# Kernel optimization log

Hardware: AMD Instinct MI355X
Metric: run time of the kernel (lower is better)

The kernel has to match this reference:

```python
import jax, jax.numpy as jnp
import numpy as np


def setup_inputs() -> dict:
    key = jax.random.key(0)
    ks = jax.random.split(key, 8)
    N, C, T, V = 32, 64, 256, 25
    OUT, INTER, S = 64, 16, 3
    W_SCALE = 0.05  # keep complex softmax exp() well-conditioned
    return {
        "x_real": jax.random.normal(ks[0], (N, C, T, V), jnp.float32),
        "x_imag": jax.random.normal(ks[1], (N, C, T, V), jnp.float32),
        "A": jax.random.uniform(ks[2], (S, V, V), jnp.float32),
        "PA": jax.random.normal(ks[3], (S, V, V), jnp.float32) * 1e-3,
        "Wa": jax.random.normal(ks[4], (S, 2 * INTER, 2 * C), jnp.float32) * W_SCALE,
        "ba": jnp.zeros((S, 2 * INTER), jnp.float32),
        "Wb": jax.random.normal(ks[5], (S, 2 * INTER, 2 * C), jnp.float32) * W_SCALE,
        "bb": jnp.zeros((S, 2 * INTER), jnp.float32),
        "Wd": jax.random.normal(ks[6], (S, 2 * OUT, 2 * C), jnp.float32) * W_SCALE,
        "bd": jnp.zeros((S, 2 * OUT), jnp.float32),
        "bn_weight": jnp.ones((OUT,), jnp.float32),
        "bn_bias": jnp.zeros((OUT,), jnp.float32),
    }


def _cconv1x1(z, W, b):
    # C_Conv2d with k=1: 1x1 conv over concat(real, imag) channels.
    zc = jnp.concatenate([z.real, z.imag], axis=1)          # [N, 2*Cin, T, V]
    o = jnp.einsum("oc,nctv->notv", W, zc) + b[None, :, None, None]
    h = W.shape[0] // 2
    return jax.lax.complex(o[:, :h], o[:, h:])              # [N, Cout, T, V] complex


def _forward(x_real, x_imag, A, PA, Wa, ba, Wb, bb, Wd, bd, bn_weight, bn_bias):
    x = jax.lax.complex(x_real, x_imag)                     # [N, C, T, V]
    N, C, T, V = x.shape
    inter = Wa.shape[1] // 2
    Afull = A + PA                                          # [3, V, V] real
    X2 = x.reshape(N, C * T, V)
    y = None
    for i in range(A.shape[0]):
        A1 = _cconv1x1(x, Wa[i], ba[i])                     # [N, inter, T, V]
        A1 = A1.transpose(0, 3, 1, 2).reshape(N, V, inter * T)
        A2 = _cconv1x1(x, Wb[i], bb[i]).reshape(N, inter * T, V)
        S = jnp.matmul(A1, A2) / (inter * T)                # [N, V, V] complex
        # complex softmax over dim=1 (no max-subtraction, faithful to C_softmax)
        ez = jnp.exp(S)
        S = ez / jnp.sum(ez, axis=1, keepdims=True)
        S = S + Afull[i]
        z = jnp.matmul(X2, S).reshape(N, C, T, V)
        z = _cconv1x1(z, Wd[i], bd[i])                      # [N, OUT, T, V]
        y = z if y is None else y + z
    # C_BatchNorm2d on complex input: complex mean, real variance = E|y-mu|^2
    mu = jnp.mean(y, axis=(0, 2, 3))                        # [OUT] complex
    var = jnp.mean(jnp.abs(y - mu[None, :, None, None]) ** 2, axis=(0, 2, 3))
    yn = (y - mu[None, :, None, None]) / jnp.sqrt(var + 1e-5)[None, :, None, None]
    yn = yn * bn_weight[None, :, None, None] + bn_bias[None, :, None, None]
    yn = yn + x  # down = identity (in_channels == out_channels)
    return jnp.stack([yn.real, yn.imag])                    # [2, N, OUT, T, V] real


def reference(x_real, x_imag, A, PA, Wa, ba, Wb, bb, Wd, bd, bn_weight, bn_bias):
    return _forward(x_real, x_imag, A, PA, Wa, ba, Wb, bb, Wd, bd, bn_weight, bn_bias)
```

## Files before the change

kernel.cpp:

```cpp
#include <hip/hip_runtime.h>
#include <hip/hip_bf16.h>
#include <stdint.h>

#define NN 32
#define CC 64
#define TTOT 256
#define VV 25
#define NS 3
constexpr int TV  = TTOT * VV;
constexpr int CTV = CC * TV;
constexpr size_t PLANE = (size_t)NN * CTV;

typedef unsigned short ushort_t;
using short8 = __attribute__((ext_vector_type(8))) short;
using f32x4  = __attribute__((ext_vector_type(4))) float;

static __device__ __forceinline__ ushort_t f2bf(float f) {
  __hip_bfloat16 h = __float2bfloat16(f);
  return reinterpret_cast<ushort_t&>(h);
}
static __device__ __forceinline__ float bf2f(ushort_t h) {
  union { uint32_t u; float f; } v; v.u = ((uint32_t)h) << 16;
  return v.f;
}
static __device__ __forceinline__ int SWZ(int row, int k) {
  return ((row << 7) + k) ^ ((row & 7) << 3);
}
static __device__ __forceinline__ int SWZ64(int row, int k) {
  return ((row << 6) + k) ^ ((row & 7) << 3);
}
static __device__ __forceinline__ f32x4 mfma16(short8 a, short8 b, f32x4 c) {
  return __builtin_amdgcn_mfma_f32_16x16x32_bf16(a, b, c, 0, 0, 0);
}
static __device__ __forceinline__ short8 negbf8(short8 x) {
  short8 r;
#pragma unroll
  for (int j = 0; j < 8; ++j) r[j] = x[j] ^ (short)0x8000;
  return r;
}

__global__ __launch_bounds__(256) void k0_wfrag(
    const float* __restrict__ Wd, const float* __restrict__ Wa,
    const float* __restrict__ Wb, ushort_t* __restrict__ wfrag,
    ushort_t* __restrict__ wab)
{
  const int i = blockIdx.x;
  for (int e = threadIdx.x; e < 16384; e += 256) {
    int ot = e >> 11, m = (e >> 9) & 3, l = (e >> 3) & 63, j = e & 7;
    int r  = ot * 16 + (l & 15);
    int c = m * 16 + ((l >> 4) << 2) + (j >> 1), comp = j & 1;
    wfrag[(size_t)i * 16384 + e] = f2bf(Wd[(size_t)i * 16384 + r * 128 + comp * 64 + c]);
  }
  for (int e = threadIdx.x; e < 8192; e += 256) {
    int mt = e >> 11, ks = (e >> 9) & 3, l = (e >> 3) & 63, j = e & 7;
    int r  = mt * 16 + (l & 15);
    int kp = ks * 32 + ((l >> 4) << 3) + j;
    float v = (r < 32) ? Wa[((size_t)i * 32 + r) * 128 + kp]
                       : Wb[((size_t)i * 32 + (r - 32)) * 128 + kp];
    wab[(size_t)i * 8192 + e] = f2bf(v);
  }
}

__global__ __launch_bounds__(256) void k1_spart(
    const float* __restrict__ xr, const float* __restrict__ xi,
    const ushort_t* __restrict__ wab, const float* __restrict__ ba,
    const float* __restrict__ bb, float* __restrict__ Spart)
{
  const int tc = blockIdx.x, n = blockIdx.y;
  const int tid = threadIdx.x, lane = tid & 63, wv = tid >> 6;
  const int r16 = lane & 15, gw = lane >> 4;
  __shared__ alignas(16) ushort_t zc[128 * 128];
  __shared__ alignas(16) ushort_t Ga[32 * 128];
  __shared__ alignas(16) ushort_t Gb[32 * 128];

  for (int e4 = tid; e4 < 128 * 25; e4 += 256) {
    int c = e4 / 25, q = e4 % 25;
    const float* src = (c < 64) ? xr : xi;
    float4 w = *(const float4*)&src[(size_t)n * CTV + (c & 63) * TV + tc * 100 + q * 4];
#pragma unroll
    for (int jj = 0; jj < 4; ++jj) {
      int g = q * 4 + jj, t = g / 25, v = g - t * 25;
      zc[SWZ(t * 32 + v, c)] = f2bf(((const float*)&w)[jj]);
    }
  }
  for (int e = tid; e < 28 * 128; e += 256) {
    int r7 = e >> 7, c = e & 127;
    int t = r7 / 7, vv = 25 + r7 % 7;
    zc[SWZ(t * 32 + vv, c)] = 0;
  }

  const int mu = wv >> 1, nv = wv & 1;

  for (int i = 0; i < NS; ++i) {
    __syncthreads();

    {
      short8 afr[4];
#pragma unroll
      for (int ks = 0; ks < 4; ++ks)
        afr[ks] = *(const short8*)&wab[((((size_t)i * 4 + wv) * 4 + ks) * 64 + lane) * 8];
      float bias[4];
#pragma unroll
      for (int j = 0; j < 4; ++j) {
        int row = wv * 16 + gw * 4 + j;
        bias[j] = (row < 32) ? ba[i * 32 + row] : bb[i * 32 + (row - 32)];
      }
      ushort_t* gbuf = (wv < 2) ? Ga : Gb;
      const int half = (wv & 1) * 64;
      for (int nt = 0; nt < 8; ++nt) {
        f32x4 acc = {0.f, 0.f, 0.f, 0.f};
        const int brow = nt * 16 + r16;
#pragma unroll
        for (int ks = 0; ks < 4; ++ks) {
          short8 bfr = *(const short8*)&zc[SWZ(brow, ks * 32 + gw * 8)];
          acc = mfma16(afr[ks], bfr, acc);
        }
        int pos2 = nt * 16 + r16;
        int t = pos2 >> 5, v = pos2 & 31;
        int k0w = half + t * 16 + gw * 4;
        uint32_t w0 = (uint32_t)f2bf(acc[0] + bias[0]) | ((uint32_t)f2bf(acc[1] + bias[1]) << 16);
        uint32_t w1 = (uint32_t)f2bf(acc[2] + bias[2]) | ((uint32_t)f2bf(acc[3] + bias[3]) << 16);
        uint2 pk; pk.x = w0; pk.y = w1;
        *(uint2*)&gbuf[SWZ(v, k0w)] = pk;
      }
    }
    __syncthreads();

    {
      const int urow = mu * 16 + r16;
      const int vrow = nv * 16 + r16;
      f32x4 Prr = {0.f,0.f,0.f,0.f}, Pii = {0.f,0.f,0.f,0.f};
      f32x4 Pri = {0.f,0.f,0.f,0.f}, Pir = {0.f,0.f,0.f,0.f};
#pragma unroll
      for (int ks = 0; ks < 2; ++ks) {
        int ko = ks * 32 + gw * 8;
        short8 arF = *(const short8*)&Ga[SWZ(urow, ko)];
        short8 aiF = *(const short8*)&Ga[SWZ(urow, 64 + ko)];
        short8 brF = *(const short8*)&Gb[SWZ(vrow, ko)];
        short8 biF = *(const short8*)&Gb[SWZ(vrow, 64 + ko)];
        Prr = mfma16(arF, brF, Prr);
        Pii = mfma16(aiF, biF, Pii);
        Pri = mfma16(arF, biF, Pri);
        Pir = mfma16(aiF, brF, Pir);
      }
#pragma unroll
      for (int j = 0; j < 4; ++j) {
        int u = mu * 16 + gw * 4 + j;
        int v = nv * 16 + r16;
        if (u < VV && v < VV) {
          size_t idx = ((((size_t)i * NN + n) * 64 + tc) * 625 + u * 25 + v) * 2;
          Spart[idx]     = Prr[j] - Pii[j];
          Spart[idx + 1] = Pri[j] + Pir[j];
        }
      }
    }
  }
}

__global__ __launch_bounds__(256) void k2_softmax(
    const float* __restrict__ Spart, const float* __restrict__ Aw,
    const float* __restrict__ PA, ushort_t* __restrict__ sfrag)
{
  const int i = blockIdx.x, n = blockIdx.y, tid = threadIdx.x;
  __shared__ float ez[625 * 2];
  __shared__ float den[25 * 2];
  for (int e = tid; e < 625; e += 256) {
    float sr = 0.f, si = 0.f;
    const float* p = Spart + (((size_t)i * NN + n) * 64 * 625 + e) * 2;
    for (int tcb = 0; tcb < 64; ++tcb) { sr += p[0]; si += p[1]; p += 625 * 2; }
    sr *= (1.f / 4096.f); si *= (1.f / 4096.f);
    float m = expf(sr);
    ez[e * 2] = m * cosf(si);
    ez[e * 2 + 1] = m * sinf(si);
  }
  __syncthreads();
  if (tid < 25) {
    float dr = 0.f, di = 0.f;
    for (int u = 0; u < 25; ++u) { dr += ez[(u * 25 + tid) * 2]; di += ez[(u * 25 + tid) * 2 + 1]; }
    float inv = 1.f / (dr * dr + di * di);
    den[tid * 2] = dr * inv; den[tid * 2 + 1] = -di * inv;
  }
  __syncthreads();
  for (int e = tid; e < 625; e += 256) {
    int v = e % 25;
    float er = ez[e * 2], ei = ez[e * 2 + 1];
    float dr = den[v * 2], di = den[v * 2 + 1];
    float outr = er * dr - ei * di + Aw[i * 625 + e] + PA[i * 625 + e];
    float outi = er * di + ei * dr;
    ez[e * 2] = outr; ez[e * 2 + 1] = outi;
  }
  __syncthreads();
  for (int e = tid; e < 256; e += 256) {
    int l = e & 63, nt = (e >> 6) & 1, m = e >> 7;
    int u0 = (l >> 4) << 3, v = nt * 16 + (l & 15);
    short8 pk;
#pragma unroll
    for (int j = 0; j < 8; ++j) {
      int u = u0 + j;
      float val = 0.f;
      if (u < VV && v < VV)
        val = (m == 0) ? ez[(u * 25 + v) * 2] : ez[(u * 25 + v) * 2 + 1];
      pk[j] = (short)f2bf(val);
    }
    *(short8*)&sfrag[((size_t)(i * NN + n) * 256 + e) * 8] = pk;
  }
}

__global__ __launch_bounds__(256, 4) void k3_y(
    const float* __restrict__ xr, const float* __restrict__ xi,
    const ushort_t* __restrict__ sfrag, const ushort_t* __restrict__ wfrag,
    const float* __restrict__ bd, float* __restrict__ out,
    float* __restrict__ bnpart)
{
  const int tq2 = blockIdx.x, n = blockIdx.y;
  const int tid = threadIdx.x, lane = tid & 63, wv = tid >> 6;
  const int r16 = lane & 15, gw = lane >> 4;
  const int tl = wv >> 1, h = wv & 1;
  __shared__ alignas(16) ushort_t xs[128 * 64];
  __shared__ float stats[4][64][2];

  for (int e2 = tid; e2 < 128 * 25; e2 += 256) {
    int c = e2 / 25, q = e2 % 25;
    const float* src = (c < 64) ? xr : xi;
    float2 w = *(const float2*)&src[(size_t)n * CTV + (size_t)(c & 63) * TV + tq2 * 50 + q * 2];
    int g0 = q * 2, g1 = g0 + 1;
    int t0 = g0 / 25, u0 = g0 - t0 * 25;
    int t1 = g1 / 25, u1 = g1 - t1 * 25;
    xs[SWZ64(c, t0 * 32 + u0)] = f2bf(w.x);
    xs[SWZ64(c, t1 * 32 + u1)] = f2bf(w.y);
  }
  for (int e = tid; e < 128 * 14; e += 256) {
    int c = e / 14, r = e % 14;
    int t = r / 7, u = 25 + r % 7;
    xs[SWZ64(c, t * 32 + u)] = 0;
  }
  __syncthreads();

  const int kx = tl * 32 + gw * 8;

  f32x4 acc[4][2];
#pragma unroll
  for (int a = 0; a < 4; ++a) { acc[a][0] = {0.f,0.f,0.f,0.f}; acc[a][1] = {0.f,0.f,0.f,0.f}; }

#pragma unroll 1
  for (int i = 0; i < NS; ++i) {
    const ushort_t* sb = sfrag + (size_t)(i * NN + n) * 2048;
    short8 sf[2][2];
#pragma unroll
    for (int m = 0; m < 2; ++m)
#pragma unroll
      for (int nt = 0; nt < 2; ++nt)
        sf[m][nt] = *(const short8*)&sb[((m * 2 + nt) * 64 + lane) * 8];

    const ushort_t* wbase = wfrag + (size_t)i * 16384;
    short8 wcur[4], wnxt[4];
#pragma unroll
    for (int m = 0; m < 4; ++m)
      wcur[m] = *(const short8*)&wbase[(size_t)(((h * 4 + 0) * 4 + m) * 64 + lane) * 8];

    short8 snI[2];
#pragma unroll
    for (int nt = 0; nt < 2; ++nt) snI[nt] = negbf8(sf[1][nt]);
    short8 bp[4][2];
#pragma unroll
    for (int tile = 0; tile < 4; ++tile) {
      short8 axr_ = *(const short8*)&xs[SWZ64(tile * 16 + r16, kx)];
      short8 axi_ = *(const short8*)&xs[SWZ64(64 + tile * 16 + r16, kx)];
#pragma unroll
      for (int nt = 0; nt < 2; ++nt) {
        f32x4 zr = {0.f,0.f,0.f,0.f}, zi = {0.f,0.f,0.f,0.f};
        zr = mfma16(axr_, sf[0][nt], zr);
        zr = mfma16(axi_, snI[nt], zr);
        zi = mfma16(axr_, sf[1][nt], zi);
        zi = mfma16(axi_, sf[0][nt], zi);
        short8 pk;
#pragma unroll
        for (int j = 0; j < 4; ++j) {
          pk[2 * j]     = (short)f2bf(zr[j]);
          pk[2 * j + 1] = (short)f2bf(zi[j]);
        }
        bp[tile][nt] = pk;
      }
    }

#pragma unroll
    for (int ot = 0; ot < 4; ++ot) {
      if (ot < 3) {
#pragma unroll
        for (int m = 0; m < 4; ++m)
          wnxt[m] = *(const short8*)&wbase[(size_t)(((h * 4 + ot + 1) * 4 + m) * 64 + lane) * 8];
      }
#pragma unroll
      for (int m = 0; m < 4; ++m) {
        acc[ot][0] = mfma16(wcur[m], bp[m][0], acc[ot][0]);
        acc[ot][1] = mfma16(wcur[m], bp[m][1], acc[ot][1]);
      }
#pragma unroll
      for (int m = 0; m < 4; ++m) wcur[m] = wnxt[m];
    }
  }

  const int t = tq2 * 2 + tl;
#pragma unroll
  for (int ot = 0; ot < 4; ++ot) {
#pragma unroll
    for (int j = 0; j < 4; ++j) {
      int lrow = ot * 16 + gw * 4 + j;
      int row = h * 64 + lrow;
      float bias = bd[row] + bd[128 + row] + bd[256 + row];
      float s = 0.f, q = 0.f;
#pragma unroll
      for (int nt = 0; nt < 2; ++nt) {
        int v = nt * 16 + r16;
        float val = acc[ot][nt][j] + bias;
        if (v < VV) {
          out[(size_t)(row >> 6) * PLANE + (size_t)n * CTV + (row & 63) * TV + t * VV + v] = val;
          s += val; q += val * val;
        }
      }
#pragma unroll
      for (int d = 1; d < 16; d <<= 1) { s += __shfl_xor(s, d); q += __shfl_xor(q, d); }
      if (r16 == 0) { stats[wv][lrow][0] = s; stats[wv][lrow][1] = q; }
    }
  }
  __syncthreads();
  if (tid < 128) {
    int hh = tid >> 6, lr = tid & 63;
    float s = stats[hh][lr][0] + stats[2 + hh][lr][0];
    float q = stats[hh][lr][1] + stats[2 + hh][lr][1];
    size_t b = (size_t)n * 128 + tq2;
    bnpart[(b * 128 + tid) * 2]     = s;
    bnpart[(b * 128 + tid) * 2 + 1] = q;
  }
}

__global__ __launch_bounds__(256) void k4_stats(
    const float* __restrict__ bnpart, const float* __restrict__ bnw,
    const float* __restrict__ bnb, float* __restrict__ coeff)
{
  const int o = blockIdx.x, tid = threadIdx.x;
  float sr = 0.f, qr = 0.f, si = 0.f, qi = 0.f;
  for (int b = tid; b < 4096; b += 256) {
    const float* p = bnpart + ((size_t)b * 128 + o) * 2;
    sr += p[0]; qr += p[1];
    const float* p2 = bnpart + ((size_t)b * 128 + 64 + o) * 2;
    si += p2[0]; qi += p2[1];
  }
#pragma unroll
  for (int d = 1; d < 64; d <<= 1) {
    sr += __shfl_xor(sr, d); qr += __shfl_xor(qr, d);
    si += __shfl_xor(si, d); qi += __shfl_xor(qi, d);
  }
  __shared__ float red[4][4];
  int lane = tid & 63, wv = tid >> 6;
  if (lane == 0) { red[wv][0] = sr; red[wv][1] = qr; red[wv][2] = si; red[wv][3] = qi; }
  __syncthreads();
  if (tid == 0) {
    sr = red[0][0] + red[1][0] + red[2][0] + red[3][0];
    qr = red[0][1] + red[1][1] + red[2][1] + red[3][1];
    si = red[0][2] + red[1][2] + red[2][2] + red[3][2];
    qi = red[0][3] + red[1][3] + red[2][3] + red[3][3];
    const float invM = 1.f / (float)((size_t)NN * TTOT * VV);
    float mur = sr * invM, mui = si * invM;
    float var = (qr + qi) * invM - mur * mur - mui * mui;
    float inv = rsqrtf(var + 1e-5f);
    coeff[o * 4 + 0] = mur; coeff[o * 4 + 1] = mui;
    coeff[o * 4 + 2] = inv * bnw[o]; coeff[o * 4 + 3] = bnb[o];
  }
}

__global__ __launch_bounds__(256) void k5_norm(
    const float* __restrict__ xr, const float* __restrict__ xi,
    const float* __restrict__ coeff, float* __restrict__ out)
{
  size_t idx0 = ((size_t)blockIdx.x * 256 + threadIdx.x) * 4;
  size_t stride = (size_t)gridDim.x * 256 * 4;
  for (size_t e = idx0; e < PLANE; e += stride) {
    int o = (int)((e / TV) & 63);
    float4 cf = *(const float4*)&coeff[o * 4];
    float4 yr = *(float4*)&out[e];
    float4 yi = *(float4*)&out[PLANE + e];
    float4 vr = *(const float4*)&xr[e];
    float4 vi = *(const float4*)&xi[e];
    yr.x = (yr.x - cf.x) * cf.z + cf.w + vr.x;
    yr.y = (yr.y - cf.x) * cf.z + cf.w + vr.y;
    yr.z = (yr.z - cf.x) * cf.z + cf.w + vr.z;
    yr.w = (yr.w - cf.x) * cf.z + cf.w + vr.w;
    yi.x = (yi.x - cf.y) * cf.z + vi.x;
    yi.y = (yi.y - cf.y) * cf.z + vi.y;
    yi.z = (yi.z - cf.y) * cf.z + vi.z;
    yi.w = (yi.w - cf.y) * cf.z + vi.w;
    *(float4*)&out[e] = yr;
    *(float4*)&out[PLANE + e] = yi;
  }
}

extern "C" void kernel_launch(void* const* d_in, const int* in_sizes, int n_in,
                              void* d_out, int out_size, void* d_ws, size_t ws_size,
                              hipStream_t stream) {
  const float* xr  = (const float*)d_in[0];
  const float* xi  = (const float*)d_in[1];
  const float* Aw  = (const float*)d_in[2];
  const float* PA  = (const float*)d_in[3];
  const float* Wa  = (const float*)d_in[4];
  const float* ba  = (const float*)d_in[5];
  const float* Wb  = (const float*)d_in[6];
  const float* bb  = (const float*)d_in[7];
  const float* Wd  = (const float*)d_in[8];
  const float* bd  = (const float*)d_in[9];
  const float* bnw = (const float*)d_in[10];
  const float* bnb = (const float*)d_in[11];
  float* out = (float*)d_out;
  float* ws = (float*)d_ws;

  float*    Spart  = ws;
  float*    bnpart = ws;
  ushort_t* sfrag  = (ushort_t*)(ws + 7680000);
  ushort_t* wfrag  = (ushort_t*)(ws + 7778304);
  ushort_t* wab    = (ushort_t*)(ws + 7802880);
  float*    coeff  = ws + 7815168;

  k0_wfrag<<<NS, 256, 0, stream>>>(Wd, Wa, Wb, wfrag, wab);
  k1_spart<<<dim3(64, NN), 256, 0, stream>>>(xr, xi, wab, ba, bb, Spart);
  k2_softmax<<<dim3(NS, NN), 256, 0, stream>>>(Spart, Aw, PA, sfrag);
  k3_y<<<dim3(128, NN), 256, 0, stream>>>(xr, xi, sfrag, wfrag, bd, out, bnpart);
  k4_stats<<<64, 256, 0, stream>>>(bnpart, bnw, bnb, coeff);
  k5_norm<<<6400, 256, 0, stream>>>(xr, xi, coeff, out);
}
```

Measured before the change: 263.8 us.

## Make k3 persistent over 8 timesteps with LDS-resident weights and double-buffered x

k3_y now runs 512-thread blocks, each covering 8 timesteps in four chunks of two instead of one block per two timesteps. The Wd fragments for all three subsets are staged once in LDS, and x chunks are prefetched into registers and written to double-buffered LDS so global loads overlap the MFMA work. k1_spart is also restructured to compute all three subsets' Ga/Gb projections before a single barrier, replacing the per-subset barrier pairs at the cost of three times the LDS for those buffers. The larger LDS footprint and register pressure may lower occupancy, and grid parallelism drops fourfold.

```diff
diff --git a/kernel.cpp b/kernel.cpp
--- a/kernel.cpp
+++ b/kernel.cpp
@@ -26,9 +26,6 @@
 static __device__ __forceinline__ int SWZ(int row, int k) {
   return ((row << 7) + k) ^ ((row & 7) << 3);
 }
-static __device__ __forceinline__ int SWZ64(int row, int k) {
-  return ((row << 6) + k) ^ ((row & 7) << 3);
-}
 static __device__ __forceinline__ f32x4 mfma16(short8 a, short8 b, f32x4 c) {
   return __builtin_amdgcn_mfma_f32_16x16x32_bf16(a, b, c, 0, 0, 0);
 }
@@ -70,8 +67,8 @@
   const int tid = threadIdx.x, lane = tid & 63, wv = tid >> 6;
   const int r16 = lane & 15, gw = lane >> 4;
   __shared__ alignas(16) ushort_t zc[128 * 128];
-  __shared__ alignas(16) ushort_t Ga[32 * 128];
-  __shared__ alignas(16) ushort_t Gb[32 * 128];
+  __shared__ alignas(16) ushort_t Ga[NS][32 * 128];
+  __shared__ alignas(16) ushort_t Gb[NS][32 * 128];
 
   for (int e4 = tid; e4 < 128 * 25; e4 += 256) {
     int c = e4 / 25, q = e4 % 25;
@@ -88,70 +85,68 @@
     int t = r7 / 7, vv = 25 + r7 % 7;
     zc[SWZ(t * 32 + vv, c)] = 0;
   }
+  __syncthreads();
+
+#pragma unroll 1
+  for (int i = 0; i < NS; ++i) {
+    short8 afr[4];
+#pragma unroll
+    for (int ks = 0; ks < 4; ++ks)
+      afr[ks] = *(const short8*)&wab[((((size_t)i * 4 + wv) * 4 + ks) * 64 + lane) * 8];
+    float bias[4];
+#pragma unroll
+    for (int j = 0; j < 4; ++j) {
+      int row = wv * 16 + gw * 4 + j;
+      bias[j] = (row < 32) ? ba[i * 32 + row] : bb[i * 32 + (row - 32)];
+    }
+    ushort_t* gbuf = (wv < 2) ? Ga[i] : Gb[i];
+    const int half = (wv & 1) * 64;
+    for (int nt = 0; nt < 8; ++nt) {
+      f32x4 acc = {0.f, 0.f, 0.f, 0.f};
+      const int brow = nt * 16 + r16;
+#pragma unroll
+      for (int ks = 0; ks < 4; ++ks) {
+        short8 bfr = *(const short8*)&zc[SWZ(brow, ks * 32 + gw * 8)];
+        acc = mfma16(afr[ks], bfr, acc);
+      }
+      int pos2 = nt * 16 + r16;
+      int t = pos2 >> 5, v = pos2 & 31;
+      int k0w = half + t * 16 + gw * 4;
+      uint32_t w0 = (uint32_t)f2bf(acc[0] + bias[0]) | ((uint32_t)f2bf(acc[1] + bias[1]) << 16);
+      uint32_t w1 = (uint32_t)f2bf(acc[2] + bias[2]) | ((uint32_t)f2bf(acc[3] + bias[3]) << 16);
+      uint2 pk; pk.x = w0; pk.y = w1;
+      *(uint2*)&gbuf[SWZ(v, k0w)] = pk;
+    }
+  }
+  __syncthreads();
 
   const int mu = wv >> 1, nv = wv & 1;
-
+  const int urow = mu * 16 + r16;
+  const int vrow = nv * 16 + r16;
+#pragma unroll 1
   for (int i = 0; i < NS; ++i) {
-    __syncthreads();
-
-    {
-      short8 afr[4];
-#pragma unroll
-      for (int ks = 0; ks < 4; ++ks)
-        afr[ks] = *(const short8*)&wab[((((size_t)i * 4 + wv) * 4 + ks) * 64 + lane) * 8];
-      float bias[4];
-#pragma unroll
-      for (int j = 0; j < 4; ++j) {
-        int row = wv * 16 + gw * 4 + j;
-        bias[j] = (row < 32) ? ba[i * 32 + row] : bb[i * 32 + (row - 32)];
-      }
-      ushort_t* gbuf = (wv < 2) ? Ga : Gb;
-      const int half = (wv & 1) * 64;
-      for (int nt = 0; nt < 8; ++nt) {
-        f32x4 acc = {0.f, 0.f, 0.f, 0.f};
-        const int brow = nt * 16 + r16;
-#pragma unroll
-        for (int ks = 0; ks < 4; ++ks) {
-          short8 bfr = *(const short8*)&zc[SWZ(brow, ks * 32 + gw * 8)];
-          acc = mfma16(afr[ks], bfr, acc);
-        }
-        int pos2 = nt * 16 + r16;
-        int t = pos2 >> 5, v = pos2 & 31;
-        int k0w = half + t * 16 + gw * 4;
-        uint32_t w0 = (uint32_t)f2bf(acc[0] + bias[0]) | ((uint32_t)f2bf(acc[1] + bias[1]) << 16);
-        uint32_t w1 = (uint32_t)f2bf(acc[2] + bias[2]) | ((uint32_t)f2bf(acc[3] + bias[3]) << 16);
-        uint2 pk; pk.x = w0; pk.y = w1;
-        *(uint2*)&gbuf[SWZ(v, k0w)] = pk;
-      }
-    }
-    __syncthreads();
-
-    {
-      const int urow = mu * 16 + r16;
-      const int vrow = nv * 16 + r16;
-      f32x4 Prr = {0.f,0.f,0.f,0.f}, Pii = {0.f,0.f,0.f,0.f};
-      f32x4 Pri = {0.f,0.f,0.f,0.f}, Pir = {0.f,0.f,0.f,0.f};
-#pragma unroll
-      for (int ks = 0; ks < 2; ++ks) {
-        int ko = ks * 32 + gw * 8;
-        short8 arF = *(const short8*)&Ga[SWZ(urow, ko)];
-        short8 aiF = *(const short8*)&Ga[SWZ(urow, 64 + ko)];
-        short8 brF = *(const short8*)&Gb[SWZ(vrow, ko)];
-        short8 biF = *(const short8*)&Gb[SWZ(vrow, 64 + ko)];
-        Prr = mfma16(arF, brF, Prr);
-        Pii = mfma16(aiF, biF, Pii);
-        Pri = mfma16(arF, biF, Pri);
-        Pir = mfma16(aiF, brF, Pir);
-      }
-#pragma unroll
-      for (int j = 0; j < 4; ++j) {
-        int u = mu * 16 + gw * 4 + j;
-        int v = nv * 16 + r16;
-        if (u < VV && v < VV) {
-          size_t idx = ((((size_t)i * NN + n) * 64 + tc) * 625 + u * 25 + v) * 2;
-          Spart[idx]     = Prr[j] - Pii[j];
-          Spart[idx + 1] = Pri[j] + Pir[j];
-        }
+    f32x4 Prr = {0.f,0.f,0.f,0.f}, Pii = {0.f,0.f,0.f,0.f};
+    f32x4 Pri = {0.f,0.f,0.f,0.f}, Pir = {0.f,0.f,0.f,0.f};
+#pragma unroll
+    for (int ks = 0; ks < 2; ++ks) {
+      int ko = ks * 32 + gw * 8;
+      short8 arF = *(const short8*)&Ga[i][SWZ(urow, ko)];
+      short8 aiF = *(const short8*)&Ga[i][SWZ(urow, 64 + ko)];
+      short8 brF = *(const short8*)&Gb[i][SWZ(vrow, ko)];
+      short8 biF = *(const short8*)&Gb[i][SWZ(vrow, 64 + ko)];
+      Prr = mfma16(arF, brF, Prr);
+      Pii = mfma16(aiF, biF, Pii);
+      Pri = mfma16(arF, biF, Pri);
+      Pir = mfma16(aiF, brF, Pir);
+    }
+#pragma unroll
+    for (int j = 0; j < 4; ++j) {
+      int u = mu * 16 + gw * 4 + j;
+      int v = nv * 16 + r16;
+      if (u < VV && v < VV) {
+        size_t idx = ((((size_t)i * NN + n) * 64 + tc) * 625 + u * 25 + v) * 2;
+        Spart[idx]     = Prr[j] - Pii[j];
+        Spart[idx + 1] = Pri[j] + Pir[j];
       }
     }
   }
@@ -206,131 +201,170 @@
   }
 }
 
-__global__ __launch_bounds__(256, 4) void k3_y(
+__global__ __launch_bounds__(512, 2) void k3_y(
     const float* __restrict__ xr, const float* __restrict__ xi,
     const ushort_t* __restrict__ sfrag, const ushort_t* __restrict__ wfrag,
     const float* __restrict__ bd, float* __restrict__ out,
     float* __restrict__ bnpart)
 {
-  const int tq2 = blockIdx.x, n = blockIdx.y;
+  const int tq8 = blockIdx.x, n = blockIdx.y;
   const int tid = threadIdx.x, lane = tid & 63, wv = tid >> 6;
   const int r16 = lane & 15, gw = lane >> 4;
-  const int tl = wv >> 1, h = wv & 1;
-  __shared__ alignas(16) ushort_t xs[128 * 64];
-  __shared__ float stats[4][64][2];
-
-  for (int e2 = tid; e2 < 128 * 25; e2 += 256) {
-    int c = e2 / 25, q = e2 % 25;
-    const float* src = (c < 64) ? xr : xi;
-    float2 w = *(const float2*)&src[(size_t)n * CTV + (size_t)(c & 63) * TV + tq2 * 50 + q * 2];
-    int g0 = q * 2, g1 = g0 + 1;
-    int t0 = g0 / 25, u0 = g0 - t0 * 25;
-    int t1 = g1 / 25, u1 = g1 - t1 * 25;
-    xs[SWZ64(c, t0 * 32 + u0)] = f2bf(w.x);
-    xs[SWZ64(c, t1 * 32 + u1)] = f2bf(w.y);
-  }
-  for (int e = tid; e < 128 * 14; e += 256) {
-    int c = e / 14, r = e % 14;
-    int t = r / 7, u = 25 + r % 7;
-    xs[SWZ64(c, t * 32 + u)] = 0;
-  }
-  __syncthreads();
-
-  const int kx = tl * 32 + gw * 8;
-
-  f32x4 acc[4][2];
-#pragma unroll
-  for (int a = 0; a < 4; ++a) { acc[a][0] = {0.f,0.f,0.f,0.f}; acc[a][1] = {0.f,0.f,0.f,0.f}; }
-
-#pragma unroll 1
+  const int tl = wv & 1, qq = wv >> 1;
+  __shared__ alignas(16) ushort_t wlds[NS * 16384];
+  __shared__ alignas(16) ushort_t xs[2][2][128][32];
+  __shared__ float stats[2][128][2];
+
+  for (int e = tid; e < 6144; e += 512)
+    *(short8*)&wlds[e * 8] = *(const short8*)&wfrag[(size_t)e * 8];
+  for (int e = tid; e < 2 * 2 * 128 * 7; e += 512) {
+    int u = 25 + (e % 7), c = (e / 7) % 128, t = (e / 896) % 2, b = e / 1792;
+    xs[b][t][c][u] = 0;
+  }
+  short8 sf[NS][2][2];
+#pragma unroll
   for (int i = 0; i < NS; ++i) {
     const ushort_t* sb = sfrag + (size_t)(i * NN + n) * 2048;
-    short8 sf[2][2];
 #pragma unroll
     for (int m = 0; m < 2; ++m)
 #pragma unroll
       for (int nt = 0; nt < 2; ++nt)
-        sf[m][nt] = *(const short8*)&sb[((m * 2 + nt) * 64 + lane) * 8];
-
-    const ushort_t* wbase = wfrag + (size_t)i * 16384;
-    short8 wcur[4], wnxt[4];
-#pragma unroll
-    for (int m = 0; m < 4; ++m)
-      wcur[m] = *(const short8*)&wbase[(size_t)(((h * 4 + 0) * 4 + m) * 64 + lane) * 8];
-
-    short8 snI[2];
-#pragma unroll
-    for (int nt = 0; nt < 2; ++nt) snI[nt] = negbf8(sf[1][nt]);
-    short8 bp[4][2];
+        sf[i][m][nt] = *(const short8*)&sb[((m * 2 + nt) * 64 + lane) * 8];
+  }
+
+  float bias[2][4];
+#pragma unroll
+  for (int o = 0; o < 2; ++o)
+#pragma unroll
+    for (int j = 0; j < 4; ++j) {
+      int row = (qq * 2 + o) * 16 + gw * 4 + j;
+      bias[o][j] = bd[row] + bd[128 + row] + bd[256 + row];
+    }
+
+  float2 px[7];
+  auto prefetch = [&](int ch) {
+#pragma unroll
+    for (int s = 0; s < 7; ++s) {
+      int e = tid + s * 512;
+      if (e < 3200) {
+        int c = e / 25, w = e % 25;
+        const float* src = (c < 64) ? xr : xi;
+        px[s] = *(const float2*)&src[(size_t)n * CTV + (size_t)(c & 63) * TV
+                                     + (tq8 * 8 + ch * 2) * 25 + w * 2];
+      }
+    }
+  };
+  prefetch(0);
+
+  float ss[2][4], qs[2][4];
+#pragma unroll
+  for (int o = 0; o < 2; ++o)
+#pragma unroll
+    for (int j = 0; j < 4; ++j) { ss[o][j] = 0.f; qs[o][j] = 0.f; }
+
+  int p = 0;
+#pragma unroll 1
+  for (int ch = 0; ch < 4; ++ch) {
+#pragma unroll
+    for (int s = 0; s < 7; ++s) {
+      int e = tid + s * 512;
+      if (e < 3200) {
+        int c = e / 25, w = e % 25;
+        int g0 = w * 2, g1 = g0 + 1;
+        xs[p][g0 / 25][c][g0 % 25] = f2bf(px[s].x);
+        xs[p][g1 / 25][c][g1 % 25] = f2bf(px[s].y);
+      }
+    }
+    if (ch < 3) prefetch(ch + 1);
+    __syncthreads();
+
+    short8 axr[4], axi_[4];
 #pragma unroll
     for (int tile = 0; tile < 4; ++tile) {
-      short8 axr_ = *(const short8*)&xs[SWZ64(tile * 16 + r16, kx)];
-      short8 axi_ = *(const short8*)&xs[SWZ64(64 + tile * 16 + r16, kx)];
-#pragma unroll
-      for (int nt = 0; nt < 2; ++nt) {
-        f32x4 zr = {0.f,0.f,0.f,0.f}, zi = {0.f,0.f,0.f,0.f};
-        zr = mfma16(axr_, sf[0][nt], zr);
-        zr = mfma16(axi_, snI[nt], zr);
-        zi = mfma16(axr_, sf[1][nt], zi);
-        zi = mfma16(axi_, sf[0][nt], zi);
-        short8 pk;
-#pragma unroll
-        for (int j = 0; j < 4; ++j) {
-          pk[2 * j]     = (short)f2bf(zr[j]);
-          pk[2 * j + 1] = (short)f2bf(zi[j]);
+      axr[tile]  = *(const short8*)&xs[p][tl][tile * 16 + r16][gw * 8];
+      axi_[tile] = *(const short8*)&xs[p][tl][64 + tile * 16 + r16][gw * 8];
+    }
+
+    f32x4 acc[2][2];
+#pragma unroll
+    for (int o = 0; o < 2; ++o) { acc[o][0] = {0.f,0.f,0.f,0.f}; acc[o][1] = {0.f,0.f,0.f,0.f}; }
+
+#pragma unroll 1
+    for (int i = 0; i < NS; ++i) {
+      short8 wreg[2][4];
+#pragma unroll
+      for (int o = 0; o < 2; ++o)
+#pragma unroll
+        for (int m = 0; m < 4; ++m)
+          wreg[o][m] = *(const short8*)&wlds[(size_t)i * 16384
+                          + (size_t)(((qq * 2 + o) * 4 + m) * 64 + lane) * 8];
+
+      short8 snI[2];
+#pragma unroll
+      for (int nt = 0; nt < 2; ++nt) snI[nt] = negbf8(sf[i][1][nt]);
+      short8 bp[4][2];
+#pragma unroll
+      for (int tile = 0; tile < 4; ++tile) {
+#pragma unroll
+        for (int nt = 0; nt < 2; ++nt) {
+          f32x4 zr = {0.f,0.f,0.f,0.f}, zi = {0.f,0.f,0.f,0.f};
+          zr = mfma16(axr[tile], sf[i][0][nt], zr);
+          zr = mfma16(axi_[tile], snI[nt], zr);
+          zi = mfma16(axr[tile], sf[i][1][nt], zi);
+          zi = mfma16(axi_[tile], sf[i][0][nt], zi);
+          short8 pk;
+#pragma unroll
+          for (int j = 0; j < 4; ++j) {
+            pk[2 * j]     = (short)f2bf(zr[j]);
+            pk[2 * j + 1] = (short)f2bf(zi[j]);
+          }
+          bp[tile][nt] = pk;
         }
-        bp[tile][nt] = pk;
-      }
-    }
-
-#pragma unroll
-    for (int ot = 0; ot < 4; ++ot) {
-      if (ot < 3) {
-#pragma unroll
-        for (int m = 0; m < 4; ++m)
-          wnxt[m] = *(const short8*)&wbase[(size_t)(((h * 4 + ot + 1) * 4 + m) * 64 + lane) * 8];
-      }
-#pragma unroll
-      for (int m = 0; m < 4; ++m) {
-        acc[ot][0] = mfma16(wcur[m], bp[m][0], acc[ot][0]);
-        acc[ot][1] = mfma16(wcur[m], bp[m][1], acc[ot][1]);
-      }
-#pragma unroll
-      for (int m = 0; m < 4; ++m) wcur[m] = wnxt[m];
-    }
-  }
-
-  const int t = tq2 * 2 + tl;
-#pragma unroll
-  for (int ot = 0; ot < 4; ++ot) {
+      }
+
+#pragma unroll
+      for (int o = 0; o < 2; ++o)
+#pragma unroll
+        for (int m = 0; m < 4; ++m) {
+          acc[o][0] = mfma16(wreg[o][m], bp[m][0], acc[o][0]);
+          acc[o][1] = mfma16(wreg[o][m], bp[m][1], acc[o][1]);
+        }
+    }
+
+    const int t = tq8 * 8 + ch * 2 + tl;
+#pragma unroll
+    for (int o = 0; o < 2; ++o)
+#pragma unroll
+      for (int j = 0; j < 4; ++j) {
+        int row = (qq * 2 + o) * 16 + gw * 4 + j;
+#pragma unroll
+        for (int nt = 0; nt < 2; ++nt) {
+          int v = nt * 16 + r16;
+          float val = acc[o][nt][j] + bias[o][j];
+          if (v < VV) {
+            out[(size_t)(row >> 6) * PLANE + (size_t)n * CTV + (row & 63) * TV + t * VV + v] = val;
+            ss[o][j] += val; qs[o][j] += val * val;
+          }
+        }
+      }
+    p ^= 1;
+  }
+
+#pragma unroll
+  for (int o = 0; o < 2; ++o)
 #pragma unroll
     for (int j = 0; j < 4; ++j) {
-      int lrow = ot * 16 + gw * 4 + j;
-      int row = h * 64 + lrow;
-      float bias = bd[row] + bd[128 + row] + bd[256 + row];
-      float s = 0.f, q = 0.f;
-#pragma unroll
-      for (int nt = 0; nt < 2; ++nt) {
-        int v = nt * 16 + r16;
-        float val = acc[ot][nt][j] + bias;
-        if (v < VV) {
-          out[(size_t)(row >> 6) * PLANE + (size_t)n * CTV + (row & 63) * TV + t * VV + v] = val;
-          s += val; q += val * val;
-        }
-      }
+      float s = ss[o][j], q = qs[o][j];
 #pragma unroll
       for (int d = 1; d < 16; d <<= 1) { s += __shfl_xor(s, d); q += __shfl_xor(q, d); }
-      if (r16 == 0) { stats[wv][lrow][0] = s; stats[wv][lrow][1] = q; }
-    }
-  }
+      int row = (qq * 2 + o) * 16 + gw * 4 + j;
+      if (r16 == 0) { stats[tl][row][0] = s; stats[tl][row][1] = q; }
+    }
   __syncthreads();
   if (tid < 128) {
-    int hh = tid >> 6, lr = tid & 63;
-    float s = stats[hh][lr][0] + stats[2 + hh][lr][0];
-    float q = stats[hh][lr][1] + stats[2 + hh][lr][1];
-    size_t b = (size_t)n * 128 + tq2;
-    bnpart[(b * 128 + tid) * 2]     = s;
-    bnpart[(b * 128 + tid) * 2 + 1] = q;
+    size_t b = (size_t)n * 32 + tq8;
+    bnpart[(b * 128 + tid) * 2]     = stats[0][tid][0] + stats[1][tid][0];
+    bnpart[(b * 128 + tid) * 2 + 1] = stats[0][tid][1] + stats[1][tid][1];
   }
 }
 
@@ -340,7 +374,7 @@
 {
   const int o = blockIdx.x, tid = threadIdx.x;
   float sr = 0.f, qr = 0.f, si = 0.f, qi = 0.f;
-  for (int b = tid; b < 4096; b += 256) {
+  for (int b = tid; b < 1024; b += 256) {
     const float* p = bnpart + ((size_t)b * 128 + o) * 2;
     sr += p[0]; qr += p[1];
     const float* p2 = bnpart + ((size_t)b * 128 + 64 + o) * 2;
@@ -423,7 +457,7 @@
   k0_wfrag<<<NS, 256, 0, stream>>>(Wd, Wa, Wb, wfrag, wab);
   k1_spart<<<dim3(64, NN), 256, 0, stream>>>(xr, xi, wab, ba, bb, Spart);
   k2_softmax<<<dim3(NS, NN), 256, 0, stream>>>(Spart, Aw, PA, sfrag);
-  k3_y<<<dim3(128, NN), 256, 0, stream>>>(xr, xi, sfrag, wfrag, bd, out, bnpart);
+  k3_y<<<dim3(32, NN), 512, 0, stream>>>(xr, xi, sfrag, wfrag, bd, out, bnpart);
   k4_stats<<<64, 256, 0, stream>>>(bnpart, bnw, bnb, coeff);
   k5_norm<<<6400, 256, 0, stream>>>(xr, xi, coeff, out);
 }
```

Measured after the change: 281.4 us. 1.07x slower.

## Stage Wd fragments in LDS and restructure k1 to batch all branches

Applied to the files above, without the earlier changes.

In k3_y, each branch's Wd weight fragments are copied cooperatively into shared memory once per block instead of every wave loading them from global memory. The x tile now uses a per-t-step layout with a simpler XOR swizzle, and the B operand is built and consumed one m-tile at a time, which shortens register live ranges. In k1_spart, the G projections for all three branches are computed before one barrier, then the S products follow, replacing two barriers per branch. The cost is more LDS per block: k3 uses about 48KB and drops its occupancy hint of 4, and k1 triples its G buffers, so fewer blocks may fit per CU.

```diff
diff --git a/kernel.cpp b/kernel.cpp
--- a/kernel.cpp
+++ b/kernel.cpp
@@ -26,9 +26,6 @@
 static __device__ __forceinline__ int SWZ(int row, int k) {
   return ((row << 7) + k) ^ ((row & 7) << 3);
 }
-static __device__ __forceinline__ int SWZ64(int row, int k) {
-  return ((row << 6) + k) ^ ((row & 7) << 3);
-}
 static __device__ __forceinline__ f32x4 mfma16(short8 a, short8 b, f32x4 c) {
   return __builtin_amdgcn_mfma_f32_16x16x32_bf16(a, b, c, 0, 0, 0);
 }
@@ -70,8 +67,8 @@
   const int tid = threadIdx.x, lane = tid & 63, wv = tid >> 6;
   const int r16 = lane & 15, gw = lane >> 4;
   __shared__ alignas(16) ushort_t zc[128 * 128];
-  __shared__ alignas(16) ushort_t Ga[32 * 128];
-  __shared__ alignas(16) ushort_t Gb[32 * 128];
+  __shared__ alignas(16) ushort_t Ga[NS][32 * 128];
+  __shared__ alignas(16) ushort_t Gb[NS][32 * 128];
 
   for (int e4 = tid; e4 < 128 * 25; e4 += 256) {
     int c = e4 / 25, q = e4 % 25;
@@ -88,70 +85,68 @@
     int t = r7 / 7, vv = 25 + r7 % 7;
     zc[SWZ(t * 32 + vv, c)] = 0;
   }
+  __syncthreads();
+
+#pragma unroll 1
+  for (int i = 0; i < NS; ++i) {
+    short8 afr[4];
+#pragma unroll
+    for (int ks = 0; ks < 4; ++ks)
+      afr[ks] = *(const short8*)&wab[((((size_t)i * 4 + wv) * 4 + ks) * 64 + lane) * 8];
+    float bias[4];
+#pragma unroll
+    for (int j = 0; j < 4; ++j) {
+      int row = wv * 16 + gw * 4 + j;
+      bias[j] = (row < 32) ? ba[i * 32 + row] : bb[i * 32 + (row - 32)];
+    }
+    ushort_t* gbuf = (wv < 2) ? Ga[i] : Gb[i];
+    const int half = (wv & 1) * 64;
+    for (int nt = 0; nt < 8; ++nt) {
+      f32x4 acc = {0.f, 0.f, 0.f, 0.f};
+      const int brow = nt * 16 + r16;
+#pragma unroll
+      for (int ks = 0; ks < 4; ++ks) {
+        short8 bfr = *(const short8*)&zc[SWZ(brow, ks * 32 + gw * 8)];
+        acc = mfma16(afr[ks], bfr, acc);
+      }
+      int pos2 = nt * 16 + r16;
+      int t = pos2 >> 5, v = pos2 & 31;
+      int k0w = half + t * 16 + gw * 4;
+      uint32_t w0 = (uint32_t)f2bf(acc[0] + bias[0]) | ((uint32_t)f2bf(acc[1] + bias[1]) << 16);
+      uint32_t w1 = (uint32_t)f2bf(acc[2] + bias[2]) | ((uint32_t)f2bf(acc[3] + bias[3]) << 16);
+      uint2 pk; pk.x = w0; pk.y = w1;
+      *(uint2*)&gbuf[SWZ(v, k0w)] = pk;
+    }
+  }
+  __syncthreads();
 
   const int mu = wv >> 1, nv = wv & 1;
-
+  const int urow = mu * 16 + r16;
+  const int vrow = nv * 16 + r16;
+#pragma unroll 1
   for (int i = 0; i < NS; ++i) {
-    __syncthreads();
-
-    {
-      short8 afr[4];
-#pragma unroll
-      for (int ks = 0; ks < 4; ++ks)
-        afr[ks] = *(const short8*)&wab[((((size_t)i * 4 + wv) * 4 + ks) * 64 + lane) * 8];
-      float bias[4];
-#pragma unroll
-      for (int j = 0; j < 4; ++j) {
-        int row = wv * 16 + gw * 4 + j;
-        bias[j] = (row < 32) ? ba[i * 32 + row] : bb[i * 32 + (row - 32)];
-      }
-      ushort_t* gbuf = (wv < 2) ? Ga : Gb;
-      const int half = (wv & 1) * 64;
-      for (int nt = 0; nt < 8; ++nt) {
-        f32x4 acc = {0.f, 0.f, 0.f, 0.f};
-        const int brow = nt * 16 + r16;
-#pragma unroll
-        for (int ks = 0; ks < 4; ++ks) {
-          short8 bfr = *(const short8*)&zc[SWZ(brow, ks * 32 + gw * 8)];
-          acc = mfma16(afr[ks], bfr, acc);
-        }
-        int pos2 = nt * 16 + r16;
-        int t = pos2 >> 5, v = pos2 & 31;
-        int k0w = half + t * 16 + gw * 4;
-        uint32_t w0 = (uint32_t)f2bf(acc[0] + bias[0]) | ((uint32_t)f2bf(acc[1] + bias[1]) << 16);
-        uint32_t w1 = (uint32_t)f2bf(acc[2] + bias[2]) | ((uint32_t)f2bf(acc[3] + bias[3]) << 16);
-        uint2 pk; pk.x = w0; pk.y = w1;
-        *(uint2*)&gbuf[SWZ(v, k0w)] = pk;
-      }
-    }
-    __syncthreads();
-
-    {
-      const int urow = mu * 16 + r16;
-      const int vrow = nv * 16 + r16;
-      f32x4 Prr = {0.f,0.f,0.f,0.f}, Pii = {0.f,0.f,0.f,0.f};
-      f32x4 Pri = {0.f,0.f,0.f,0.f}, Pir = {0.f,0.f,0.f,0.f};
-#pragma unroll
-      for (int ks = 0; ks < 2; ++ks) {
-        int ko = ks * 32 + gw * 8;
-        short8 arF = *(const short8*)&Ga[SWZ(urow, ko)];
-        short8 aiF = *(const short8*)&Ga[SWZ(urow, 64 + ko)];
-        short8 brF = *(const short8*)&Gb[SWZ(vrow, ko)];
-        short8 biF = *(const short8*)&Gb[SWZ(vrow, 64 + ko)];
-        Prr = mfma16(arF, brF, Prr);
-        Pii = mfma16(aiF, biF, Pii);
-        Pri = mfma16(arF, biF, Pri);
-        Pir = mfma16(aiF, brF, Pir);
-      }
-#pragma unroll
-      for (int j = 0; j < 4; ++j) {
-        int u = mu * 16 + gw * 4 + j;
-        int v = nv * 16 + r16;
-        if (u < VV && v < VV) {
-          size_t idx = ((((size_t)i * NN + n) * 64 + tc) * 625 + u * 25 + v) * 2;
-          Spart[idx]     = Prr[j] - Pii[j];
-          Spart[idx + 1] = Pri[j] + Pir[j];
-        }
+    f32x4 Prr = {0.f,0.f,0.f,0.f}, Pii = {0.f,0.f,0.f,0.f};
+    f32x4 Pri = {0.f,0.f,0.f,0.f}, Pir = {0.f,0.f,0.f,0.f};
+#pragma unroll
+    for (int ks = 0; ks < 2; ++ks) {
+      int ko = ks * 32 + gw * 8;
+      short8 arF = *(const short8*)&Ga[i][SWZ(urow, ko)];
+      short8 aiF = *(const short8*)&Ga[i][SWZ(urow, 64 + ko)];
+      short8 brF = *(const short8*)&Gb[i][SWZ(vrow, ko)];
+      short8 biF = *(const short8*)&Gb[i][SWZ(vrow, 64 + ko)];
+      Prr = mfma16(arF, brF, Prr);
+      Pii = mfma16(aiF, biF, Pii);
+      Pri = mfma16(arF, biF, Pri);
+      Pir = mfma16(aiF, brF, Pir);
+    }
+#pragma unroll
+    for (int j = 0; j < 4; ++j) {
+      int u = mu * 16 + gw * 4 + j;
+      int v = nv * 16 + r16;
+      if (u < VV && v < VV) {
+        size_t idx = ((((size_t)i * NN + n) * 64 + tc) * 625 + u * 25 + v) * 2;
+        Spart[idx]     = Prr[j] - Pii[j];
+        Spart[idx + 1] = Pri[j] + Pir[j];
       }
     }
   }
@@ -206,7 +201,7 @@
   }
 }
 
-__global__ __launch_bounds__(256, 4) void k3_y(
+__global__ __launch_bounds__(256) void k3_y(
     const float* __restrict__ xr, const float* __restrict__ xi,
     const ushort_t* __restrict__ sfrag, const ushort_t* __restrict__ wfrag,
     const float* __restrict__ bd, float* __restrict__ out,
@@ -216,7 +211,8 @@
   const int tid = threadIdx.x, lane = tid & 63, wv = tid >> 6;
   const int r16 = lane & 15, gw = lane >> 4;
   const int tl = wv >> 1, h = wv & 1;
-  __shared__ alignas(16) ushort_t xs[128 * 64];
+  __shared__ alignas(16) ushort_t xs[2][4096];
+  __shared__ alignas(16) ushort_t wbuf[16384];
   __shared__ float stats[4][64][2];
 
   for (int e2 = tid; e2 < 128 * 25; e2 += 256) {
@@ -226,17 +222,15 @@
     int g0 = q * 2, g1 = g0 + 1;
     int t0 = g0 / 25, u0 = g0 - t0 * 25;
     int t1 = g1 / 25, u1 = g1 - t1 * 25;
-    xs[SWZ64(c, t0 * 32 + u0)] = f2bf(w.x);
-    xs[SWZ64(c, t1 * 32 + u1)] = f2bf(w.y);
+    int sw = (c & 3) << 3;
+    xs[t0][c * 32 + (u0 ^ sw)] = f2bf(w.x);
+    xs[t1][c * 32 + (u1 ^ sw)] = f2bf(w.y);
   }
   for (int e = tid; e < 128 * 14; e += 256) {
     int c = e / 14, r = e % 14;
     int t = r / 7, u = 25 + r % 7;
-    xs[SWZ64(c, t * 32 + u)] = 0;
-  }
-  __syncthreads();
-
-  const int kx = tl * 32 + gw * 8;
+    xs[t][c * 32 + (u ^ ((c & 3) << 3))] = 0;
+  }
 
   f32x4 acc[4][2];
 #pragma unroll
@@ -244,6 +238,12 @@
 
 #pragma unroll 1
   for (int i = 0; i < NS; ++i) {
+    __syncthreads();
+
+    short8 tmp[8];
+#pragma unroll
+    for (int q = 0; q < 8; ++q)
+      tmp[q] = *(const short8*)&wfrag[(size_t)i * 16384 + (size_t)(q * 256 + tid) * 8];
     const ushort_t* sb = sfrag + (size_t)(i * NN + n) * 2048;
     short8 sf[2][2];
 #pragma unroll
@@ -251,21 +251,22 @@
 #pragma unroll
       for (int nt = 0; nt < 2; ++nt)
         sf[m][nt] = *(const short8*)&sb[((m * 2 + nt) * 64 + lane) * 8];
-
-    const ushort_t* wbase = wfrag + (size_t)i * 16384;
-    short8 wcur[4], wnxt[4];
-#pragma unroll
-    for (int m = 0; m < 4; ++m)
-      wcur[m] = *(const short8*)&wbase[(size_t)(((h * 4 + 0) * 4 + m) * 64 + lane) * 8];
+#pragma unroll
+    for (int q = 0; q < 8; ++q)
+      *(short8*)&wbuf[(q * 256 + tid) * 8] = tmp[q];
+    __syncthreads();
 
     short8 snI[2];
 #pragma unroll
     for (int nt = 0; nt < 2; ++nt) snI[nt] = negbf8(sf[1][nt]);
-    short8 bp[4][2];
-#pragma unroll
-    for (int tile = 0; tile < 4; ++tile) {
-      short8 axr_ = *(const short8*)&xs[SWZ64(tile * 16 + r16, kx)];
-      short8 axi_ = *(const short8*)&xs[SWZ64(64 + tile * 16 + r16, kx)];
+
+#pragma unroll
+    for (int m = 0; m < 4; ++m) {
+      int cr = m * 16 + r16;
+      int ko = (gw * 8) ^ ((r16 & 3) << 3);
+      short8 axr_ = *(const short8*)&xs[tl][cr * 32 + ko];
+      short8 axi_ = *(const short8*)&xs[tl][(64 + cr) * 32 + ko];
+      short8 bp[2];
 #pragma unroll
       for (int nt = 0; nt < 2; ++nt) {
         f32x4 zr = {0.f,0.f,0.f,0.f}, zi = {0.f,0.f,0.f,0.f};
@@ -279,40 +280,31 @@
           pk[2 * j]     = (short)f2bf(zr[j]);
           pk[2 * j + 1] = (short)f2bf(zi[j]);
         }
-        bp[tile][nt] = pk;
+        bp[nt] = pk;
       }
-    }
-
-#pragma unroll
-    for (int ot = 0; ot < 4; ++ot) {
-      if (ot < 3) {
-#pragma unroll
-        for (int m = 0; m < 4; ++m)
-          wnxt[m] = *(const short8*)&wbase[(size_t)(((h * 4 + ot + 1) * 4 + m) * 64 + lane) * 8];
+#pragma unroll
+      for (int otl = 0; otl < 4; ++otl) {
+        int ot = h * 4 + otl;
+        short8 a = *(const short8*)&wbuf[(size_t)((ot * 4 + m) * 64 + lane) * 8];
+        acc[otl][0] = mfma16(a, bp[0], acc[otl][0]);
+        acc[otl][1] = mfma16(a, bp[1], acc[otl][1]);
       }
-#pragma unroll
-      for (int m = 0; m < 4; ++m) {
-        acc[ot][0] = mfma16(wcur[m], bp[m][0], acc[ot][0]);
-        acc[ot][1] = mfma16(wcur[m], bp[m][1], acc[ot][1]);
-      }
-#pragma unroll
-      for (int m = 0; m < 4; ++m) wcur[m] = wnxt[m];
     }
   }
 
   const int t = tq2 * 2 + tl;
 #pragma unroll
-  for (int ot = 0; ot < 4; ++ot) {
+  for (int otl = 0; otl < 4; ++otl) {
 #pragma unroll
     for (int j = 0; j < 4; ++j) {
-      int lrow = ot * 16 + gw * 4 + j;
+      int lrow = otl * 16 + gw * 4 + j;
       int row = h * 64 + lrow;
       float bias = bd[row] + bd[128 + row] + bd[256 + row];
       float s = 0.f, q = 0.f;
 #pragma unroll
       for (int nt = 0; nt < 2; ++nt) {
         int v = nt * 16 + r16;
-        float val = acc[ot][nt][j] + bias;
+        float val = acc[otl][nt][j] + bias;
         if (v < VV) {
           out[(size_t)(row >> 6) * PLANE + (size_t)n * CTV + (row & 63) * TV + t * VV + v] = val;
           s += val; q += val * val;
```

Result: faster. 256.6 us (-2.7%).
